# Performance work log

Measured on AMD Instinct MI355X. Metric: run time of the kernel, lower is better.

The kernel has to match this reference:

```python
import jax, jax.numpy as jnp
import numpy as np

N_NODES = 100000
N_EDGES = 1600000
D = 128


def setup_inputs() -> dict:
    key = jax.random.key(0)
    ks = jax.random.split(key, 10)
    s = 1.0 / np.sqrt(D)
    return {
        "feat": jax.random.normal(ks[0], (N_NODES, D), dtype=jnp.float32),
        "W_self0": jax.random.normal(ks[1], (D, D), dtype=jnp.float32) * s,
        "W_neigh0": jax.random.normal(ks[2], (D, D), dtype=jnp.float32) * s,
        "b0": jnp.zeros((D,), dtype=jnp.float32),
        "W_self1": jax.random.normal(ks[3], (D, D), dtype=jnp.float32) * s,
        "W_neigh1": jax.random.normal(ks[4], (D, D), dtype=jnp.float32) * s,
        "b1": jnp.zeros((D,), dtype=jnp.float32),
        "ln_g": jnp.ones((D,), dtype=jnp.float32),
        "ln_b": jnp.zeros((D,), dtype=jnp.float32),
        "edge_src": jax.random.randint(ks[5], (N_EDGES,), 0, N_NODES, dtype=jnp.int32),
        "edge_dst": jax.random.randint(ks[6], (N_EDGES,), 0, N_NODES, dtype=jnp.int32),
        "in_deg": jax.random.randint(ks[7], (N_NODES,), 1, 64, dtype=jnp.int32),
    }


def _sage_layer(h, src, dst, inv_deg, W_self, W_neigh, b):
    # mean aggregation over incoming neighbors: gather -> segment_sum -> scale
    msg = jax.ops.segment_sum(h[src], dst, num_segments=N_NODES)  # [N, d]
    h_neigh = msg * inv_deg[:, None]
    return h @ W_self + h_neigh @ W_neigh + b


def _layer_norm(x, g, b, eps=1e-5):
    mu = jnp.mean(x, axis=-1, keepdims=True)
    var = jnp.mean((x - mu) ** 2, axis=-1, keepdims=True)
    return (x - mu) * jax.lax.rsqrt(var + eps) * g + b


def reference(feat, W_self0, W_neigh0, b0, W_self1, W_neigh1, b1, ln_g, ln_b,
              edge_src, edge_dst, in_deg):
    # Eval mode: dropout = identity, no EmbeddingSelector / reg loss.
    inv_deg = 1.0 / jnp.maximum(in_deg, 1).astype(feat.dtype)
    h = _sage_layer(feat, edge_src, edge_dst, inv_deg, W_self0, W_neigh0, b0)
    h = _layer_norm(h, ln_g, ln_b)
    h = jax.nn.relu(h)
    h = _sage_layer(h, edge_src, edge_dst, inv_deg, W_self1, W_neigh1, b1)
    return h
```

## Files before the change

### kernel.cpp

```cpp
#include <hip/hip_runtime.h>

#define D 128
#define NN 100000
#define PB 391
#define EPB 4096

typedef __attribute__((ext_vector_type(8))) short short8;
typedef __attribute__((ext_vector_type(16))) float floatx16;
typedef __attribute__((ext_vector_type(2))) float floatx2;

__device__ inline unsigned short bf16_rne(float f) {
    unsigned int u = __float_as_uint(f);
    u += 0x7fff + ((u >> 16) & 1);
    return (unsigned short)(u >> 16);
}
__device__ inline unsigned char fp8_enc1(float f) {
    return (unsigned char)(__builtin_amdgcn_cvt_pk_fp8_f32(f, f, 0, false) & 0xff);
}

__global__ __launch_bounds__(256) void prep_kernel(
    const float* __restrict__ feat, unsigned short* __restrict__ feat16,
    unsigned char* __restrict__ feat8,
    const float* __restrict__ Ws0, const float* __restrict__ Wn0,
    const float* __restrict__ Ws1, const float* __restrict__ Wn1,
    unsigned short* __restrict__ wt0, unsigned short* __restrict__ wt1)
{
    int bid = blockIdx.x;
    if (bid < 12500) {
        int i = bid * 256 + threadIdx.x;
        float4 v = *(const float4*)(feat + (size_t)i * 4);
        unsigned short u[4] = { bf16_rne(v.x), bf16_rne(v.y), bf16_rne(v.z), bf16_rne(v.w) };
        *(uint2*)(feat16 + (size_t)i * 4) = *(uint2*)u;
        int w = __builtin_amdgcn_cvt_pk_fp8_f32(v.x, v.y, 0, false);
        w = __builtin_amdgcn_cvt_pk_fp8_f32(v.z, v.w, w, true);
        ((unsigned int*)feat8)[i] = (unsigned int)w;
    } else {
        int i = (bid - 12500) * 256 + threadIdx.x;
        int layer = i >> 15;
        int r = i & 32767;
        int n = r >> 8;
        int k = r & 255;
        const float* Ws = layer ? Ws1 : Ws0;
        const float* Wn = layer ? Wn1 : Wn0;
        float v = (k < 128) ? Ws[(size_t)k * 128 + n] : Wn[(size_t)(k - 128) * 128 + n];
        unsigned short* wt = layer ? wt1 : wt0;
        wt[(size_t)n * 256 + k] = bf16_rne(v);
    }
}

__global__ __launch_bounds__(256) void part_count_kernel(
    const int* __restrict__ dst, unsigned int* __restrict__ bucketCnt,
    unsigned int* __restrict__ blockBase, int E)
{
    __shared__ unsigned int h[PB];
    const int t = threadIdx.x;
    const int b = blockIdx.x;
    for (int i = t; i < PB; i += 256) h[i] = 0;
    __syncthreads();
    const int base = b * EPB;
#pragma unroll
    for (int k = 0; k < EPB / 256; k++) {
        int e = base + k * 256 + t;
        if (e < E) atomicAdd(&h[(unsigned)dst[e] >> 8], 1u);
    }
    __syncthreads();
    for (int i = t; i < PB; i += 256) {
        unsigned int c = h[i];
        unsigned int o = 0;
        if (c) o = atomicAdd(&bucketCnt[i], c);
        blockBase[(size_t)b * PB + i] = o;
    }
}

__global__ __launch_bounds__(512) void part_scan_kernel(
    const unsigned int* __restrict__ bucketCnt, unsigned int* __restrict__ bucketStart,
    int E)
{
    __shared__ unsigned int sd[512];
    int t = threadIdx.x;
    unsigned int v = (t < PB) ? bucketCnt[t] : 0u;
    sd[t] = v; __syncthreads();
    for (int off = 1; off < 512; off <<= 1) {
        unsigned int x = (t >= off) ? sd[t - off] : 0u;
        __syncthreads();
        sd[t] += x;
        __syncthreads();
    }
    if (t < PB) bucketStart[t] = sd[t] - v;
    if (t == 0) bucketStart[PB] = (unsigned int)E;
}

__global__ __launch_bounds__(256) void part_scatter_kernel(
    const int* __restrict__ src, const int* __restrict__ dst,
    const unsigned int* __restrict__ bucketStart,
    const unsigned int* __restrict__ blockBase,
    unsigned int* __restrict__ pairs, int E)
{
    __shared__ unsigned int h[PB];
    const int t = threadIdx.x;
    const int b = blockIdx.x;
    for (int i = t; i < PB; i += 256) h[i] = 0;
    __syncthreads();
    const int base = b * EPB;
#pragma unroll
    for (int k = 0; k < EPB / 256; k++) {
        int e = base + k * 256 + t;
        if (e < E) {
            unsigned int d = (unsigned int)dst[e];
            unsigned int bk = d >> 8;
            unsigned int lr = atomicAdd(&h[bk], 1u);
            unsigned int pos = bucketStart[bk] + blockBase[(size_t)b * PB + bk] + lr;
            pairs[pos] = ((unsigned int)src[e] << 8) | (d & 255u);
        }
    }
}

__global__ __launch_bounds__(256) void part_fine_kernel(
    const unsigned int* __restrict__ pairs, const unsigned int* __restrict__ bucketStart,
    int* __restrict__ row_ptr, int* __restrict__ col, int N, int E)
{
    __shared__ unsigned int h[256], sc[256], pos[256];
    const int t = threadIdx.x;
    const int b = blockIdx.x;
    h[t] = 0;
    __syncthreads();
    const unsigned int ebeg = bucketStart[b];
    const unsigned int eend = bucketStart[b + 1];
    for (unsigned int i = ebeg + t; i < eend; i += 256)
        atomicAdd(&h[pairs[i] & 255u], 1u);
    __syncthreads();
    sc[t] = h[t]; __syncthreads();
    for (int off = 1; off < 256; off <<= 1) {
        unsigned int x = (t >= off) ? sc[t - off] : 0u;
        __syncthreads();
        sc[t] += x;
        __syncthreads();
    }
    unsigned int excl = sc[t] - h[t];
    int node = b * 256 + t;
    if (node < N) row_ptr[node] = (int)(ebeg + excl);
    pos[t] = ebeg + excl;
    if (b == 0 && t == 0) row_ptr[N] = E;
    __syncthreads();
    for (unsigned int i = ebeg + t; i < eend; i += 256) {
        unsigned int p = pairs[i];
        unsigned int w = atomicAdd(&pos[p & 255u], 1u);
        col[w] = (int)(p >> 8);
    }
}

__global__ __launch_bounds__(256) void gather8_kernel(
    const unsigned char* __restrict__ h8, const int* __restrict__ row_ptr,
    const int* __restrict__ col, const int* __restrict__ in_deg,
    unsigned short* __restrict__ msg16, int N)
{
    const int wave = threadIdx.x >> 6;
    const int lane = threadIdx.x & 63;
    const int quad = lane >> 4;
    const int ln16 = lane & 15;
    const int node = (blockIdx.x * 4 + wave) * 4 + quad;
    if (node >= N) return;

    const size_t lo = (size_t)ln16 * 8;
    int beg = row_ptr[node];
    int end = row_ptr[node + 1];

    float f[8] = {0.f,0.f,0.f,0.f,0.f,0.f,0.f,0.f};
    int j = beg;
    for (; j + 4 <= end; j += 4) {
        int c0 = col[j], c1 = col[j + 1], c2 = col[j + 2], c3 = col[j + 3];
        uint2 u0 = *(const uint2*)(h8 + (size_t)c0 * D + lo);
        uint2 u1 = *(const uint2*)(h8 + (size_t)c1 * D + lo);
        uint2 u2 = *(const uint2*)(h8 + (size_t)c2 * D + lo);
        uint2 u3 = *(const uint2*)(h8 + (size_t)c3 * D + lo);
#pragma unroll
        for (int q = 0; q < 4; q++) {
            uint2 u = q == 0 ? u0 : q == 1 ? u1 : q == 2 ? u2 : u3;
            floatx2 p0 = __builtin_amdgcn_cvt_pk_f32_fp8((int)u.x, false);
            floatx2 p1 = __builtin_amdgcn_cvt_pk_f32_fp8((int)u.x, true);
            floatx2 p2 = __builtin_amdgcn_cvt_pk_f32_fp8((int)u.y, false);
            floatx2 p3 = __builtin_amdgcn_cvt_pk_f32_fp8((int)u.y, true);
            f[0] += p0.x; f[1] += p0.y; f[2] += p1.x; f[3] += p1.y;
            f[4] += p2.x; f[5] += p2.y; f[6] += p3.x; f[7] += p3.y;
        }
    }
    for (; j < end; ++j) {
        uint2 u = *(const uint2*)(h8 + (size_t)col[j] * D + lo);
        floatx2 p0 = __builtin_amdgcn_cvt_pk_f32_fp8((int)u.x, false);
        floatx2 p1 = __builtin_amdgcn_cvt_pk_f32_fp8((int)u.x, true);
        floatx2 p2 = __builtin_amdgcn_cvt_pk_f32_fp8((int)u.y, false);
        floatx2 p3 = __builtin_amdgcn_cvt_pk_f32_fp8((int)u.y, true);
        f[0] += p0.x; f[1] += p0.y; f[2] += p1.x; f[3] += p1.y;
        f[4] += p2.x; f[5] += p2.y; f[6] += p3.x; f[7] += p3.y;
    }
    int dg = in_deg[node];
    float invd = 1.f / (float)(dg > 1 ? dg : 1);
    unsigned short us[8];
#pragma unroll
    for (int i = 0; i < 8; i++) us[i] = bf16_rne(f[i] * invd);
    *(uint4*)(msg16 + (size_t)node * D + ln16 * 8) = *(const uint4*)us;
}

__global__ __launch_bounds__(256) void mfma32_kernel(
    const unsigned short* __restrict__ A16, const unsigned short* __restrict__ Msg16,
    const unsigned short* __restrict__ Wt,
    const float* __restrict__ bias,
    const float* __restrict__ ln_g, const float* __restrict__ ln_b,
    unsigned short* __restrict__ Out16, unsigned char* __restrict__ Out8,
    float* __restrict__ Out32, int N, int do_ln)
{
    __shared__ unsigned short sB[32768];

    const int tid  = threadIdx.x;
    const int wave = tid >> 6;
    const int lane = tid & 63;
    const int half = lane >> 5;
    const int n32  = lane & 31;
    const int wrow0 = blockIdx.x * 128 + wave * 32;

#pragma unroll
    for (int i = 0; i < 16; i++) {
        int idx = tid + i * 256;
        int n = idx & 127;
        int c = idx >> 7;
        uint4 w = *(const uint4*)(Wt + (size_t)n * 256 + c * 8);
        int hs = c >> 4, kc = (c >> 1) & 7, hf = c & 1;
        int ct = n >> 5, nn = n & 31;
        int chunk = (((ct * 2 + hs) * 8 + kc) * 2 + hf) * 32 + nn;
        *(uint4*)&sB[(size_t)chunk * 8] = w;
    }
    __syncthreads();

    const int arow = wrow0 + n32;
    const bool arv = arow < N;
    const size_t koff = (size_t)half * 8;

    floatx16 acc[4];
#pragma unroll
    for (int ct = 0; ct < 4; ct++)
#pragma unroll
        for (int r = 0; r < 16; r++) acc[ct][r] = 0.f;

#pragma unroll
    for (int hs = 0; hs < 2; hs++) {
        const unsigned short* Asrc = hs ? Msg16 : A16;
#pragma unroll
        for (int kc = 0; kc < 8; kc++) {
            short8 a;
            if (arv) a = *(const short8*)(Asrc + (size_t)arow * D + kc * 16 + koff);
            else     a = (short8){0,0,0,0,0,0,0,0};
#pragma unroll
            for (int ct = 0; ct < 4; ct++) {
                short8 b = *(const short8*)&sB[((size_t)((ct * 2 + hs) * 8 + kc) * 64 + lane) * 8];
                acc[ct] = __builtin_amdgcn_mfma_f32_32x32x16_bf16(a, b, acc[ct], 0, 0, 0);
            }
        }
    }

    float bb[4];
#pragma unroll
    for (int ct = 0; ct < 4; ct++) bb[ct] = bias[ct * 32 + n32];

    float v[4][16];
#pragma unroll
    for (int ct = 0; ct < 4; ct++)
#pragma unroll
        for (int r = 0; r < 16; r++) v[ct][r] = acc[ct][r] + bb[ct];

    if (do_ln) {
        float gg[4], be[4];
#pragma unroll
        for (int ct = 0; ct < 4; ct++) {
            gg[ct] = ln_g[ct * 32 + n32];
            be[ct] = ln_b[ct * 32 + n32];
        }
        float s[16], s2[16];
#pragma unroll
        for (int r = 0; r < 16; r++) {
            s[r]  = v[0][r] + v[1][r] + v[2][r] + v[3][r];
            s2[r] = v[0][r]*v[0][r] + v[1][r]*v[1][r] + v[2][r]*v[2][r] + v[3][r]*v[3][r];
        }
#pragma unroll
        for (int off = 1; off < 32; off <<= 1) {
#pragma unroll
            for (int r = 0; r < 16; r++) {
                s[r]  += __shfl_xor(s[r],  off);
                s2[r] += __shfl_xor(s2[r], off);
            }
        }
#pragma unroll
        for (int r = 0; r < 16; r++) {
            float mean = s[r] * (1.f / 128.f);
            float var  = s2[r] * (1.f / 128.f) - mean * mean;
            float rstd = rsqrtf(var + 1e-5f);
            int row_g = wrow0 + (r & 3) + 8 * (r >> 2) + 4 * half;
            if (row_g < N) {
#pragma unroll
                for (int ct = 0; ct < 4; ct++) {
                    float t = (v[ct][r] - mean) * rstd * gg[ct] + be[ct];
                    t = t > 0.f ? t : 0.f;
                    Out16[(size_t)row_g * D + ct * 32 + n32] = bf16_rne(t);
                    Out8[(size_t)row_g * D + ct * 32 + n32] = fp8_enc1(t);
                }
            }
        }
    } else {
#pragma unroll
        for (int r = 0; r < 16; r++) {
            int row_g = wrow0 + (r & 3) + 8 * (r >> 2) + 4 * half;
            if (row_g < N) {
#pragma unroll
                for (int ct = 0; ct < 4; ct++)
                    Out32[(size_t)row_g * D + ct * 32 + n32] = v[ct][r];
            }
        }
    }
}

extern "C" void kernel_launch(void* const* d_in, const int* in_sizes, int n_in,
                              void* d_out, int out_size, void* d_ws, size_t ws_size,
                              hipStream_t stream)
{
    const float* feat = (const float*)d_in[0];
    const float* Ws0  = (const float*)d_in[1];
    const float* Wn0  = (const float*)d_in[2];
    const float* b0   = (const float*)d_in[3];
    const float* Ws1  = (const float*)d_in[4];
    const float* Wn1  = (const float*)d_in[5];
    const float* b1   = (const float*)d_in[6];
    const float* lng  = (const float*)d_in[7];
    const float* lnb  = (const float*)d_in[8];
    const int* esrc   = (const int*)d_in[9];
    const int* edst   = (const int*)d_in[10];
    const int* indeg  = (const int*)d_in[11];

    const int N = NN;
    const int E = in_sizes[9];

    float* out = (float*)d_out;

    const int nblk = (E + EPB - 1) / EPB;
    char* ws = (char*)d_ws;
    size_t o = 0;
    auto alloc = [&](size_t bytes) { char* p = ws + o; o += (bytes + 15) & ~(size_t)15; return p; };
    unsigned short* feat16 = (unsigned short*)alloc((size_t)N * D * 2);
    int* col     = (int*)alloc((size_t)E * 4);
    int* row_ptr = (int*)alloc((size_t)(N + 1) * 4);
    unsigned short* wt0 = (unsigned short*)alloc(128 * 256 * 2);
    unsigned short* wt1 = (unsigned short*)alloc(128 * 256 * 2);
    size_t csr_bytes = (size_t)(512 + 512 + (size_t)nblk * PB + E) * 4 + 64;
    char* regD = alloc((size_t)N * D * 2 > csr_bytes ? (size_t)N * D * 2 : csr_bytes);
    unsigned int* bucketCnt   = (unsigned int*)regD;
    unsigned int* bucketStart = bucketCnt + 512;
    unsigned int* blockBase   = bucketStart + 512;
    unsigned int* pairs       = blockBase + (size_t)nblk * PB;
    unsigned short* h116 = (unsigned short*)regD;

    unsigned short* msg0  = (unsigned short*)d_out;
    unsigned char*  feat8 = (unsigned char*)d_out + (size_t)N * D * 2;
    unsigned char*  h18   = (unsigned char*)d_out + (size_t)N * D * 3;
    unsigned short* msg1  = feat16;
    (void)ws_size;

    const int gemm_blocks = (N + 127) / 128;
    const int gather_blocks = (N + 15) / 16;

    prep_kernel<<<12500 + 256, 256, 0, stream>>>(
        feat, feat16, feat8, Ws0, Wn0, Ws1, Wn1, wt0, wt1);

    hipMemsetAsync(bucketCnt, 0, 512 * 4, stream);
    part_count_kernel<<<nblk, 256, 0, stream>>>(edst, bucketCnt, blockBase, E);
    part_scan_kernel<<<1, 512, 0, stream>>>(bucketCnt, bucketStart, E);
    part_scatter_kernel<<<nblk, 256, 0, stream>>>(esrc, edst, bucketStart, blockBase, pairs, E);
    part_fine_kernel<<<PB, 256, 0, stream>>>(pairs, bucketStart, row_ptr, col, N, E);

    gather8_kernel<<<gather_blocks, 256, 0, stream>>>(feat8, row_ptr, col, indeg, msg0, N);
    mfma32_kernel<<<gemm_blocks, 256, 0, stream>>>(
        feat16, msg0, wt0, b0, lng, lnb, h116, h18, nullptr, N, 1);

    gather8_kernel<<<gather_blocks, 256, 0, stream>>>(h18, row_ptr, col, indeg, msg1, N);
    mfma32_kernel<<<gemm_blocks, 256, 0, stream>>>(
        h116, msg1, wt1, b1, nullptr, nullptr, nullptr, nullptr, out, N, 0);
}
```

Before: 319.7 us.

## Fuse prep with edge-count kernel and stage GEMM outputs through LDS for coalesced stores

```diff
diff --git a/kernel.cpp b/kernel.cpp
--- a/kernel.cpp
+++ b/kernel.cpp
@@ -4,6 +4,7 @@
 #define NN 100000
 #define PB 391
 #define EPB 4096
+#define PREP_BLKS 12756
 
 typedef __attribute__((ext_vector_type(8))) short short8;
 typedef __attribute__((ext_vector_type(16))) float floatx16;
@@ -18,13 +19,16 @@
     return (unsigned char)(__builtin_amdgcn_cvt_pk_fp8_f32(f, f, 0, false) & 0xff);
 }
 
-__global__ __launch_bounds__(256) void prep_kernel(
+__global__ __launch_bounds__(256) void prep_count_kernel(
     const float* __restrict__ feat, unsigned short* __restrict__ feat16,
     unsigned char* __restrict__ feat8,
     const float* __restrict__ Ws0, const float* __restrict__ Wn0,
     const float* __restrict__ Ws1, const float* __restrict__ Wn1,
-    unsigned short* __restrict__ wt0, unsigned short* __restrict__ wt1)
-{
+    unsigned short* __restrict__ wt0, unsigned short* __restrict__ wt1,
+    const int* __restrict__ dst, unsigned int* __restrict__ bucketCnt,
+    unsigned int* __restrict__ blockBase, int E)
+{
+    __shared__ unsigned int h[PB];
     int bid = blockIdx.x;
     if (bid < 12500) {
         int i = bid * 256 + threadIdx.x;
@@ -34,7 +38,7 @@
         int w = __builtin_amdgcn_cvt_pk_fp8_f32(v.x, v.y, 0, false);
         w = __builtin_amdgcn_cvt_pk_fp8_f32(v.z, v.w, w, true);
         ((unsigned int*)feat8)[i] = (unsigned int)w;
-    } else {
+    } else if (bid < PREP_BLKS) {
         int i = (bid - 12500) * 256 + threadIdx.x;
         int layer = i >> 15;
         int r = i & 32767;
@@ -45,30 +49,24 @@
         float v = (k < 128) ? Ws[(size_t)k * 128 + n] : Wn[(size_t)(k - 128) * 128 + n];
         unsigned short* wt = layer ? wt1 : wt0;
         wt[(size_t)n * 256 + k] = bf16_rne(v);
-    }
-}
-
-__global__ __launch_bounds__(256) void part_count_kernel(
-    const int* __restrict__ dst, unsigned int* __restrict__ bucketCnt,
-    unsigned int* __restrict__ blockBase, int E)
-{
-    __shared__ unsigned int h[PB];
-    const int t = threadIdx.x;
-    const int b = blockIdx.x;
-    for (int i = t; i < PB; i += 256) h[i] = 0;
-    __syncthreads();
-    const int base = b * EPB;
-#pragma unroll
-    for (int k = 0; k < EPB / 256; k++) {
-        int e = base + k * 256 + t;
-        if (e < E) atomicAdd(&h[(unsigned)dst[e] >> 8], 1u);
-    }
-    __syncthreads();
-    for (int i = t; i < PB; i += 256) {
-        unsigned int c = h[i];
-        unsigned int o = 0;
-        if (c) o = atomicAdd(&bucketCnt[i], c);
-        blockBase[(size_t)b * PB + i] = o;
+    } else {
+        const int b = bid - PREP_BLKS;
+        const int t = threadIdx.x;
+        for (int i = t; i < PB; i += 256) h[i] = 0;
+        __syncthreads();
+        const int base = b * EPB;
+#pragma unroll
+        for (int k = 0; k < EPB / 256; k++) {
+            int e = base + k * 256 + t;
+            if (e < E) atomicAdd(&h[(unsigned)dst[e] >> 8], 1u);
+        }
+        __syncthreads();
+        for (int i = t; i < PB; i += 256) {
+            unsigned int c = h[i];
+            unsigned int o = 0;
+            if (c) o = atomicAdd(&bucketCnt[i], c);
+            blockBase[(size_t)b * PB + i] = o;
+        }
     }
 }
 
@@ -216,7 +214,8 @@
     const int lane = tid & 63;
     const int half = lane >> 5;
     const int n32  = lane & 31;
-    const int wrow0 = blockIdx.x * 128 + wave * 32;
+    const int brow0 = blockIdx.x * 128;
+    const int wrow0 = brow0 + wave * 32;
 
 #pragma unroll
     for (int i = 0; i < 16; i++) {
@@ -267,6 +266,8 @@
 #pragma unroll
         for (int r = 0; r < 16; r++) v[ct][r] = acc[ct][r] + bb[ct];
 
+    __syncthreads();
+
     if (do_ln) {
         float gg[4], be[4];
 #pragma unroll
@@ -288,31 +289,50 @@
                 s2[r] += __shfl_xor(s2[r], off);
             }
         }
+        unsigned short* sO16 = sB;
+        unsigned char*  sO8  = (unsigned char*)sB + 32768;
 #pragma unroll
         for (int r = 0; r < 16; r++) {
             float mean = s[r] * (1.f / 128.f);
             float var  = s2[r] * (1.f / 128.f) - mean * mean;
             float rstd = rsqrtf(var + 1e-5f);
-            int row_g = wrow0 + (r & 3) + 8 * (r >> 2) + 4 * half;
-            if (row_g < N) {
-#pragma unroll
-                for (int ct = 0; ct < 4; ct++) {
-                    float t = (v[ct][r] - mean) * rstd * gg[ct] + be[ct];
-                    t = t > 0.f ? t : 0.f;
-                    Out16[(size_t)row_g * D + ct * 32 + n32] = bf16_rne(t);
-                    Out8[(size_t)row_g * D + ct * 32 + n32] = fp8_enc1(t);
-                }
+            int brow = wave * 32 + (r & 3) + 8 * (r >> 2) + 4 * half;
+#pragma unroll
+            for (int ct = 0; ct < 4; ct++) {
+                float t = (v[ct][r] - mean) * rstd * gg[ct] + be[ct];
+                t = t > 0.f ? t : 0.f;
+                sO16[brow * 128 + ct * 32 + n32] = bf16_rne(t);
+                sO8 [brow * 128 + ct * 32 + n32] = fp8_enc1(t);
             }
         }
+        __syncthreads();
+#pragma unroll
+        for (int i = 0; i < 8; i++) {
+            int ch = tid + i * 256;
+            if (brow0 + (ch >> 4) < N)
+                *(uint4*)(Out16 + (size_t)brow0 * D + ch * 8) = *(const uint4*)&sO16[ch * 8];
+        }
+#pragma unroll
+        for (int i = 0; i < 4; i++) {
+            int ch = tid + i * 256;
+            if (brow0 + (ch >> 3) < N)
+                *(uint4*)(Out8 + (size_t)brow0 * D + ch * 16) = *(const uint4*)&sO8[ch * 16];
+        }
     } else {
+        float* sO32 = (float*)sB;
 #pragma unroll
         for (int r = 0; r < 16; r++) {
-            int row_g = wrow0 + (r & 3) + 8 * (r >> 2) + 4 * half;
-            if (row_g < N) {
-#pragma unroll
-                for (int ct = 0; ct < 4; ct++)
-                    Out32[(size_t)row_g * D + ct * 32 + n32] = v[ct][r];
-            }
+            int brow = wave * 32 + (r & 3) + 8 * (r >> 2) + 4 * half;
+#pragma unroll
+            for (int ct = 0; ct < 4; ct++)
+                sO32[brow * 128 + ct * 32 + n32] = v[ct][r];
+        }
+        __syncthreads();
+#pragma unroll
+        for (int i = 0; i < 16; i++) {
+            int ch = tid + i * 256;
+            if (brow0 + (ch >> 5) < N)
+                *(uint4*)(Out32 + (size_t)brow0 * D + ch * 4) = *(const uint4*)&sO32[ch * 4];
         }
     }
 }
@@ -365,11 +385,11 @@
     const int gemm_blocks = (N + 127) / 128;
     const int gather_blocks = (N + 15) / 16;
 
-    prep_kernel<<<12500 + 256, 256, 0, stream>>>(
-        feat, feat16, feat8, Ws0, Wn0, Ws1, Wn1, wt0, wt1);
-
     hipMemsetAsync(bucketCnt, 0, 512 * 4, stream);
-    part_count_kernel<<<nblk, 256, 0, stream>>>(edst, bucketCnt, blockBase, E);
+    prep_count_kernel<<<PREP_BLKS + nblk, 256, 0, stream>>>(
+        feat, feat16, feat8, Ws0, Wn0, Ws1, Wn1, wt0, wt1,
+        edst, bucketCnt, blockBase, E);
+
     part_scan_kernel<<<1, 512, 0, stream>>>(bucketCnt, bucketStart, E);
     part_scatter_kernel<<<nblk, 256, 0, stream>>>(esrc, edst, bucketStart, blockBase, pairs, E);
     part_fine_kernel<<<PB, 256, 0, stream>>>(pairs, bucketStart, row_ptr, col, N, E);
```

New measurement: 315.8 us. Within noise of the previous version (-1.2%).
